# Kernel tuning notes

Measured on AMD Instinct MI355X. Metric: run time of the kernel, lower is better.

The kernel has to match this reference:

```python
import jax, jax.numpy as jnp
import numpy as np

CLASS_NUM = 31
KERNEL_MUL = 2.0
KERNEL_NUM = 5


def setup_inputs() -> dict:
    key = jax.random.key(0)
    k1, k2, k3, k4 = jax.random.split(key, 4)
    B, D = 4096, 512
    source = jax.random.normal(k1, (B, D), dtype=jnp.float32)
    target = jax.random.normal(k2, (B, D), dtype=jnp.float32)
    s_label = jax.random.randint(k3, (B,), 0, CLASS_NUM)
    t_label = jax.random.uniform(k4, (B, CLASS_NUM), dtype=jnp.float32)
    return {"source": source, "target": target, "s_label": s_label, "t_label": t_label}


def _cal_weight(s_label, t_label):
    # Faithful port of the numpy weight computation (detached in the original).
    C = CLASS_NUM
    s_onehot = jax.nn.one_hot(s_label, C, dtype=jnp.float32)          # [Bs, C]
    s_sum = s_onehot.sum(axis=0)
    s_vec = s_onehot / jnp.where(s_sum == 0, 1e9, s_sum)
    t_pred = jnp.argmax(t_label, axis=1)
    t_sum = t_label.sum(axis=0)
    t_vec = t_label / jnp.where(t_sum == 0, 1.0, t_sum)
    # classes present in BOTH source labels and target argmax predictions
    s_present = s_onehot.sum(axis=0) > 0
    t_present = jax.nn.one_hot(t_pred, C, dtype=jnp.float32).sum(axis=0) > 0
    mask = (s_present & t_present).astype(jnp.float32)                # [C]
    s_vec = s_vec * mask
    t_vec = t_vec * mask
    length = mask.sum()
    inv_len = jnp.where(length > 0, 1.0 / length, 0.0)
    w_ss = (s_vec @ s_vec.T) * inv_len
    w_tt = (t_vec @ t_vec.T) * inv_len
    w_st = (s_vec @ t_vec.T) * inv_len
    w_ts = (t_vec @ s_vec.T) * inv_len
    return w_ss, w_tt, w_st, w_ts


def _gaussian_kernel(source, target):
    n = source.shape[0] + target.shape[0]
    total = jnp.concatenate([source, target], axis=0)                 # [n, d]
    # Gram-matrix trick for pairwise squared L2 (avoids n x n x d intermediate)
    sq = jnp.sum(total * total, axis=1)                               # [n]
    L2 = jnp.maximum(sq[:, None] + sq[None, :] - 2.0 * (total @ total.T), 0.0)
    bandwidth = jax.lax.stop_gradient(jnp.sum(L2)) / (n * n - n)      # .data -> detach
    bandwidth = bandwidth / (KERNEL_MUL ** (KERNEL_NUM // 2))
    kernels = jnp.zeros_like(L2)
    for i in range(KERNEL_NUM):
        kernels = kernels + jnp.exp(-L2 / (bandwidth * KERNEL_MUL ** i))
    return kernels


def reference(source, target, s_label, t_label):
    B = source.shape[0]
    w_ss, w_tt, w_st, w_ts = _cal_weight(s_label, t_label)
    w_ss = jax.lax.stop_gradient(w_ss)
    w_tt = jax.lax.stop_gradient(w_tt)
    w_st = jax.lax.stop_gradient(w_st)
    w_ts = jax.lax.stop_gradient(w_ts)
    kernels = _gaussian_kernel(source, target)
    SS = kernels[:B, :B]
    TT = kernels[B:, B:]
    ST = kernels[:B, B:]
    TS = kernels[B:, :B]
    loss = (jnp.sum(w_ss * SS) + jnp.sum(w_tt * TT)
            - jnp.sum(w_st * ST) - jnp.sum(w_ts * TS))
    # original returns 0 if the kernel matrix contains NaNs
    return jnp.where(jnp.any(jnp.isnan(kernels)), 0.0, loss)
```

## Files before the change

### kernel.cpp

```cpp
#include <hip/hip_runtime.h>

#define N_TOT 8192
#define BHALF 4096
#define D 512
#define C 31
#define NKCI 4
#define QS 21.166666666666668f
#define C2 0.0044644089288178575f

typedef float f32x16 __attribute__((ext_vector_type(16)));
typedef int   i32x16 __attribute__((ext_vector_type(16)));
typedef int   i32x4  __attribute__((ext_vector_type(4)));
typedef __bf16 bf16x8 __attribute__((ext_vector_type(8)));

__device__ __forceinline__ uint bf16_rne(uint u) {
  return (u + 0x7fffu + ((u >> 16) & 1u)) >> 16;
}
__device__ __forceinline__ void split2(float x, uint& h, uint& lo) {
  uint u = __float_as_uint(x);
  h = bf16_rne(u);
  float hf = __uint_as_float(h << 16);
  lo = bf16_rne(__float_as_uint(x - hf));
}
__device__ __forceinline__ void gll16(const void* g, void* s) {
  __builtin_amdgcn_global_load_lds(
      (const __attribute__((address_space(1))) unsigned int*)g,
      (__attribute__((address_space(3))) unsigned int*)s, 16, 0, 0);
}
__device__ __forceinline__ uint pack4(const float* x, int o) {
  uint r = 0;
  #pragma unroll
  for (int b = 0; b < 4; ++b) {
    float xs = x[o + b] * QS;
    xs = fmaxf(fminf(xs, 127.f), -127.f);
    int q = __float2int_rn(xs);
    r |= (uint)(q & 255) << (8 * b);
  }
  return r;
}

__global__ __launch_bounds__(256) void k_split(const float* __restrict__ src,
                                               const float* __restrict__ tgt,
                                               const float* __restrict__ tl,
                                               uchar* __restrict__ qG,
                                               float* __restrict__ sq,
                                               float* __restrict__ m,
                                               float* __restrict__ tsum,
                                               int* __restrict__ pres) {
  __shared__ float lsq[4][32];
  __shared__ float lcol[128];
  __shared__ float ts[C];
  int tid = threadIdx.x, l = tid & 63, wid = tid >> 6;
  int bx = (int)blockIdx.x;
  if (bx < 1024) {
    int rg = bx >> 2;
    int kb = bx & 3;
    int ksg = kb * 4 + wid;
    int row = rg * 32 + (l & 31);
    int k0 = ksg * 32 + (l >> 5) * 16;
    const float* p = (row < BHALF) ? src + (size_t)row * D : tgt + (size_t)(row - BHALF) * D;
    float x[16];
    #pragma unroll
    for (int q = 0; q < 4; ++q) {
      float4 v = *(const float4*)(p + k0 + q * 4);
      x[q*4+0] = v.x; x[q*4+1] = v.y; x[q*4+2] = v.z; x[q*4+3] = v.w;
    }
    uint4 o = make_uint4(pack4(x, 0), pack4(x, 4), pack4(x, 8), pack4(x, 12));
    *(uint4*)(qG + (((size_t)rg * 16 + ksg) * 64 + l) * 16) = o;
    float s = 0.f;
    #pragma unroll
    for (int j = 0; j < 16; ++j) s = fmaf(x[j], x[j], s);
    s += __shfl_xor(s, 32);
    if (l < 32) lsq[wid][l] = s;
    #pragma unroll
    for (int off = 1; off <= 16; off <<= 1)
      #pragma unroll
      for (int j = 0; j < 16; ++j) x[j] += __shfl_xor(x[j], off);
    if ((l & 31) == 0) {
      #pragma unroll
      for (int j = 0; j < 16; ++j) lcol[wid * 32 + (l >> 5) * 16 + j] = x[j];
    }
    __syncthreads();
    if (tid < 32) {
      float t = lsq[0][tid] + lsq[1][tid] + lsq[2][tid] + lsq[3][tid];
      atomicAdd(&sq[rg * 32 + tid], t);
    } else if (tid >= 128) {
      int cc = tid - 128;
      atomicAdd(&m[kb * 128 + cc], lcol[cc]);
    }
  } else {
    int b = bx - 1024;
    if (tid < C) ts[tid] = 0.f;
    __syncthreads();
    int base = b * 128 * C;
    for (int idx = tid; idx < 128 * C; idx += 256) {
      atomicAdd(&ts[idx % C], tl[base + idx]);
    }
    if (tid < 128) {
      int row = b * 128 + tid;
      const float* p = tl + (size_t)row * C;
      float best = p[0]; int bi = 0;
      for (int c = 1; c < C; c++) { float v = p[c]; if (v > best) { best = v; bi = c; } }
      pres[bi] = 1;
    }
    __syncthreads();
    if (tid < C) atomicAdd(&tsum[tid], ts[tid]);
  }
}

__global__ __launch_bounds__(256) void k_prep(const float* __restrict__ sq,
                                              const float* __restrict__ m,
                                              const int* __restrict__ slab,
                                              const float* __restrict__ tsum,
                                              const int* __restrict__ pres,
                                              float* __restrict__ sval,
                                              float* __restrict__ tscale,
                                              float* __restrict__ scal,
                                              float* __restrict__ out) {
  __shared__ float red[4];
  __shared__ int cnt[C];
  __shared__ float Ssh, Msh;
  int tid = threadIdx.x;
  if (tid < C) cnt[tid] = 0;
  float s = 0.f;
  for (int i = tid; i < N_TOT; i += 256) s += sq[i];
  #pragma unroll
  for (int off = 32; off; off >>= 1) s += __shfl_xor(s, off);
  if ((tid & 63) == 0) red[tid >> 6] = s;
  __syncthreads();
  if (tid == 0) Ssh = red[0] + red[1] + red[2] + red[3];
  __syncthreads();
  float q = 0.f;
  for (int d = tid; d < D; d += 256) q += m[d] * m[d];
  #pragma unroll
  for (int off = 32; off; off >>= 1) q += __shfl_xor(q, off);
  if ((tid & 63) == 0) red[tid >> 6] = q;
  __syncthreads();
  if (tid == 0) Msh = red[0] + red[1] + red[2] + red[3];
  for (int i = tid; i < BHALF; i += 256) atomicAdd(&cnt[slab[i]], 1);
  __syncthreads();
  if (tid == 0) {
    double S = (double)Ssh, M2 = (double)Msh;
    double sumL2 = 2.0 * (double)N_TOT * S - 2.0 * M2;
    double bw = sumL2 / ((double)N_TOT * (double)N_TOT - (double)N_TOT) / 4.0;
    scal[0] = (float)(-1.4426950408889634 / (16.0 * bw));
    int len = 0;
    for (int c = 0; c < C; c++) {
      int mk = (cnt[c] > 0 && pres[c] != 0) ? 1 : 0;
      len += mk;
      sval[c] = mk ? (1.0f / (float)cnt[c]) : 0.0f;
      float tv = tsum[c];
      tscale[c] = mk ? (1.0f / (tv == 0.0f ? 1.0f : tv)) : 0.0f;
    }
    scal[1] = (len > 0) ? (1.0f / (float)len) : 0.0f;
    out[0] = 0.f;
  }
}

__global__ __launch_bounds__(256, 4) void k_main(
    const uchar* __restrict__ qG,
    const int* __restrict__ slab, const float* __restrict__ tl,
    const float* __restrict__ sval, const float* __restrict__ tscale,
    const float* __restrict__ sq, const float* __restrict__ scal,
    float* __restrict__ out) {
  __shared__ uint4 As4[1024];
  __shared__ uint4 Bs4[1024];
  __shared__ float sqA[128], sqB[128], red[4];
  uchar* As = (uchar*)As4;
  uchar* Bs = (uchar*)Bs4;
  ushort* AsU = (ushort*)As4;
  ushort* BsU = (ushort*)Bs4;

  int tid = threadIdx.x;
  int l = tid & 63, wid = tid >> 6;

  int bid = (int)blockIdx.x;
  int swz = (bid & 7) * 260 + (bid >> 3);

  int ti = 0, rem = swz;
  for (;;) { int w = 64 - ti; if (rem < w) break; rem -= w; ++ti; }
  int tj = ti + rem;

  if (tid < 128) { sqA[tid] = sq[ti * 128 + tid]; sqB[tid] = sq[tj * 128 + tid]; }
  float nib = scal[0], invlen = scal[1];

  i32x16 zeroi;
  f32x16 zero16;
  #pragma unroll
  for (int k = 0; k < 16; ++k) { zeroi[k] = 0; zero16[k] = 0.f; }
  i32x16 acc[2][2];
  acc[0][0] = zeroi; acc[0][1] = zeroi; acc[1][0] = zeroi; acc[1][1] = zeroi;

  int wrg = (wid >> 1) * 2;
  int wcg = (wid & 1) * 2;

  int rgbase_m = ((wid < 2) ? ti : tj) * 4;
  int rg_off = (wid & 1) * 2;
  uchar* lb_m = (wid < 2) ? As : Bs;

  for (int kci = 0; kci < NKCI; ++kci) {
    #pragma unroll
    for (int r = 0; r < 8; ++r) {
      int rgl = rg_off + (r >> 2), ksl = r & 3;
      const uchar* g = qG + (((size_t)(rgbase_m + rgl) * 16 + kci * 4 + ksl) * 64 + l) * 16;
      gll16(g, lb_m + ((rgl * 4 + ksl) * 64 + l) * 16);
    }
    __syncthreads();
    __builtin_amdgcn_s_setprio(1);
    #pragma unroll
    for (int ksl = 0; ksl < 4; ++ksl) {
      i32x4 a0 = *(const i32x4*)(As + (((wrg + 0) * 4 + ksl) * 64 + l) * 16);
      i32x4 a1 = *(const i32x4*)(As + (((wrg + 1) * 4 + ksl) * 64 + l) * 16);
      i32x4 b0 = *(const i32x4*)(Bs + (((wcg + 0) * 4 + ksl) * 64 + l) * 16);
      i32x4 b1 = *(const i32x4*)(Bs + (((wcg + 1) * 4 + ksl) * 64 + l) * 16);
      acc[0][0] = __builtin_amdgcn_mfma_i32_32x32x32_i8(a0, b0, acc[0][0], 0, 0, 0);
      acc[0][1] = __builtin_amdgcn_mfma_i32_32x32x32_i8(a0, b1, acc[0][1], 0, 0, 0);
      acc[1][0] = __builtin_amdgcn_mfma_i32_32x32x32_i8(a1, b0, acc[1][0], 0, 0, 0);
      acc[1][1] = __builtin_amdgcn_mfma_i32_32x32x32_i8(a1, b1, acc[1][1], 0, 0, 0);
    }
    __builtin_amdgcn_s_setprio(0);
    __syncthreads();
  }

  #pragma unroll
  for (int it = 0; it < 4; ++it) {
    int slot = tid + it * 256;
    int pl = slot >> 6;
    int ll = slot & 63;
    int side = pl >> 3;
    int rgl = (pl & 7) >> 1;
    int ks = pl & 1;
    int row = (side ? tj : ti) * 128 + rgl * 32 + (ll & 31);
    int j0 = ks * 16 + (ll >> 5) * 8;
    float vals[8];
    if (row < BHALF) {
      int cls = slab[row];
      float v = sval[cls];
      #pragma unroll
      for (int jj = 0; jj < 8; ++jj) vals[jj] = (j0 + jj == cls) ? v : 0.f;
    } else {
      const float* p = tl + (size_t)(row - BHALF) * C;
      #pragma unroll
      for (int jj = 0; jj < 8; ++jj) {
        int cj = j0 + jj;
        vals[jj] = (cj < C) ? -p[cj] * tscale[cj] : 0.f;
      }
    }
    uint h[8], lo[8];
    #pragma unroll
    for (int jj = 0; jj < 8; ++jj) split2(vals[jj], h[jj], lo[jj]);
    ushort* base = (side ? BsU : AsU) + ((rgl * 2 + ks) * 64 + ll) * 8;
    *(uint4*)base = make_uint4(h[0]|(h[1]<<16), h[2]|(h[3]<<16),
                               h[4]|(h[5]<<16), h[6]|(h[7]<<16));
    *(uint4*)(base + 4096) = make_uint4(lo[0]|(lo[1]<<16), lo[2]|(lo[3]<<16),
                                        lo[4]|(lo[5]<<16), lo[6]|(lo[7]<<16));
  }
  __syncthreads();

  float partial = 0.f;
  int colb = (wid & 1) * 64 + (l & 31);
  int rowb = (wid >> 1) * 64 + 4 * (l >> 5);
  #pragma unroll
  for (int i = 0; i < 2; ++i) {
    bf16x8 caH0 = *(const bf16x8*)(AsU + (((wrg + i) * 2 + 0) * 64 + l) * 8);
    bf16x8 caH1 = *(const bf16x8*)(AsU + (((wrg + i) * 2 + 1) * 64 + l) * 8);
    bf16x8 caL0 = *(const bf16x8*)(AsU + 4096 + (((wrg + i) * 2 + 0) * 64 + l) * 8);
    bf16x8 caL1 = *(const bf16x8*)(AsU + 4096 + (((wrg + i) * 2 + 1) * 64 + l) * 8);
    #pragma unroll
    for (int j = 0; j < 2; ++j) {
      bf16x8 cbH0 = *(const bf16x8*)(BsU + (((wcg + j) * 2 + 0) * 64 + l) * 8);
      bf16x8 cbH1 = *(const bf16x8*)(BsU + (((wcg + j) * 2 + 1) * 64 + l) * 8);
      bf16x8 cbL0 = *(const bf16x8*)(BsU + 4096 + (((wcg + j) * 2 + 0) * 64 + l) * 8);
      bf16x8 cbL1 = *(const bf16x8*)(BsU + 4096 + (((wcg + j) * 2 + 1) * 64 + l) * 8);
      f32x16 w = zero16;
      w = __builtin_amdgcn_mfma_f32_32x32x16_bf16(caH0, cbH0, w, 0, 0, 0);
      w = __builtin_amdgcn_mfma_f32_32x32x16_bf16(caH1, cbH1, w, 0, 0, 0);
      w = __builtin_amdgcn_mfma_f32_32x32x16_bf16(caH0, cbL0, w, 0, 0, 0);
      w = __builtin_amdgcn_mfma_f32_32x32x16_bf16(caH1, cbL1, w, 0, 0, 0);
      w = __builtin_amdgcn_mfma_f32_32x32x16_bf16(caL0, cbH0, w, 0, 0, 0);
      w = __builtin_amdgcn_mfma_f32_32x32x16_bf16(caL1, cbH1, w, 0, 0, 0);
      float sb = sqB[colb + j * 32];
      #pragma unroll
      for (int reg = 0; reg < 16; ++reg) {
        int row = rowb + i * 32 + (reg & 3) + 8 * (reg >> 2);
        float l2 = fmaxf(sqA[row] + sb - C2 * (float)acc[i][j][reg], 0.f);
        float e = __builtin_amdgcn_exp2f(l2 * nib);
        float kern = e;
        e *= e; kern += e;
        e *= e; kern += e;
        e *= e; kern += e;
        e *= e; kern += e;
        partial = fmaf(w[reg], kern, partial);
      }
    }
  }
  #pragma unroll
  for (int off = 32; off; off >>= 1) partial += __shfl_xor(partial, off);
  if (l == 0) red[wid] = partial;
  __syncthreads();
  if (tid == 0) {
    float v = (red[0] + red[1] + red[2] + red[3]) * invlen * ((ti == tj) ? 1.0f : 2.0f);
    atomicAdd(out, v);
  }
}

extern "C" void kernel_launch(void* const* d_in, const int* in_sizes, int n_in,
                              void* d_out, int out_size, void* d_ws, size_t ws_size,
                              hipStream_t stream) {
  const float* src = (const float*)d_in[0];
  const float* tgt = (const float*)d_in[1];
  const int* slab  = (const int*)d_in[2];
  const float* tl  = (const float*)d_in[3];
  float* out = (float*)d_out;

  uchar*  qG = (uchar*)d_ws;
  float* fb  = (float*)(qG + 4194304);
  float* sq     = fb;
  float* m      = fb + 8192;
  float* tsum   = fb + 8704;
  int*   pres   = (int*)(fb + 8736);
  float* sval   = fb + 8768;
  float* tscale = fb + 8800;
  float* scal   = fb + 8832;

  hipMemsetAsync(fb, 0, 8864 * sizeof(float), stream);
  hipLaunchKernelGGL(k_split, dim3(1056), dim3(256), 0, stream,
                     src, tgt, tl, qG, sq, m, tsum, pres);
  hipLaunchKernelGGL(k_prep,  dim3(1),    dim3(256), 0, stream,
                     sq, m, slab, tsum, pres, sval, tscale, scal, out);
  hipLaunchKernelGGL(k_main,  dim3(2080), dim3(256), 0, stream,
                     qG, slab, tl, sval, tscale, sq, scal, out);
}
```

Measured before the change: 93.76 us.

## Double-buffer k_main loads and fold prep kernel into split and main

Removes the single-block k_prep launch: class counts move into k_split's label blocks, and every k_main block recomputes the bandwidth and class weights redundantly after its GEMM loop. The K loop of k_main now uses two LDS buffers with smaller k-steps, issuing the next stage's async global-to-LDS loads before computing on the current one, with explicit vmcnt waits and raw barriers instead of __syncthreads. This is meant to hide load latency and cut one serial launch. In exchange each of the 2080 blocks rereads and reduces the 8192-entry sq array and the m vector.

```diff
diff --git a/kernel.cpp b/kernel.cpp
--- a/kernel.cpp
+++ b/kernel.cpp
@@ -4,7 +4,6 @@
 #define BHALF 4096
 #define D 512
 #define C 31
-#define NKCI 4
 #define QS 21.166666666666668f
 #define C2 0.0044644089288178575f
 
@@ -42,14 +41,18 @@
 __global__ __launch_bounds__(256) void k_split(const float* __restrict__ src,
                                                const float* __restrict__ tgt,
                                                const float* __restrict__ tl,
+                                               const int* __restrict__ slab,
                                                uchar* __restrict__ qG,
                                                float* __restrict__ sq,
                                                float* __restrict__ m,
                                                float* __restrict__ tsum,
-                                               int* __restrict__ pres) {
+                                               int* __restrict__ pres,
+                                               int* __restrict__ cnt,
+                                               float* __restrict__ out) {
   __shared__ float lsq[4][32];
   __shared__ float lcol[128];
   __shared__ float ts[C];
+  __shared__ int hcnt[C];
   int tid = threadIdx.x, l = tid & 63, wid = tid >> 6;
   int bx = (int)blockIdx.x;
   if (bx < 1024) {
@@ -90,7 +93,7 @@
     }
   } else {
     int b = bx - 1024;
-    if (tid < C) ts[tid] = 0.f;
+    if (tid < C) { ts[tid] = 0.f; hcnt[tid] = 0; }
     __syncthreads();
     int base = b * 128 * C;
     for (int idx = tid; idx < 128 * C; idx += 256) {
@@ -102,88 +105,40 @@
       float best = p[0]; int bi = 0;
       for (int c = 1; c < C; c++) { float v = p[c]; if (v > best) { best = v; bi = c; } }
       pres[bi] = 1;
-    }
+      atomicAdd(&hcnt[slab[row]], 1);
+    }
+    if (b == 0 && tid == 255) out[0] = 0.f;
     __syncthreads();
-    if (tid < C) atomicAdd(&tsum[tid], ts[tid]);
-  }
-}
-
-__global__ __launch_bounds__(256) void k_prep(const float* __restrict__ sq,
-                                              const float* __restrict__ m,
-                                              const int* __restrict__ slab,
-                                              const float* __restrict__ tsum,
-                                              const int* __restrict__ pres,
-                                              float* __restrict__ sval,
-                                              float* __restrict__ tscale,
-                                              float* __restrict__ scal,
-                                              float* __restrict__ out) {
-  __shared__ float red[4];
-  __shared__ int cnt[C];
-  __shared__ float Ssh, Msh;
-  int tid = threadIdx.x;
-  if (tid < C) cnt[tid] = 0;
-  float s = 0.f;
-  for (int i = tid; i < N_TOT; i += 256) s += sq[i];
-  #pragma unroll
-  for (int off = 32; off; off >>= 1) s += __shfl_xor(s, off);
-  if ((tid & 63) == 0) red[tid >> 6] = s;
-  __syncthreads();
-  if (tid == 0) Ssh = red[0] + red[1] + red[2] + red[3];
-  __syncthreads();
-  float q = 0.f;
-  for (int d = tid; d < D; d += 256) q += m[d] * m[d];
-  #pragma unroll
-  for (int off = 32; off; off >>= 1) q += __shfl_xor(q, off);
-  if ((tid & 63) == 0) red[tid >> 6] = q;
-  __syncthreads();
-  if (tid == 0) Msh = red[0] + red[1] + red[2] + red[3];
-  for (int i = tid; i < BHALF; i += 256) atomicAdd(&cnt[slab[i]], 1);
-  __syncthreads();
-  if (tid == 0) {
-    double S = (double)Ssh, M2 = (double)Msh;
-    double sumL2 = 2.0 * (double)N_TOT * S - 2.0 * M2;
-    double bw = sumL2 / ((double)N_TOT * (double)N_TOT - (double)N_TOT) / 4.0;
-    scal[0] = (float)(-1.4426950408889634 / (16.0 * bw));
-    int len = 0;
-    for (int c = 0; c < C; c++) {
-      int mk = (cnt[c] > 0 && pres[c] != 0) ? 1 : 0;
-      len += mk;
-      sval[c] = mk ? (1.0f / (float)cnt[c]) : 0.0f;
-      float tv = tsum[c];
-      tscale[c] = mk ? (1.0f / (tv == 0.0f ? 1.0f : tv)) : 0.0f;
-    }
-    scal[1] = (len > 0) ? (1.0f / (float)len) : 0.0f;
-    out[0] = 0.f;
-  }
-}
+    if (tid < C) {
+      atomicAdd(&tsum[tid], ts[tid]);
+      atomicAdd(&cnt[tid], hcnt[tid]);
+    }
+  }
+}
+
+#define WAITV4 asm volatile("s_waitcnt vmcnt(4)" ::: "memory")
+#define WAITV0 asm volatile("s_waitcnt vmcnt(0)" ::: "memory")
+#define WAITL0 asm volatile("s_waitcnt lgkmcnt(0)" ::: "memory")
 
 __global__ __launch_bounds__(256, 4) void k_main(
     const uchar* __restrict__ qG,
     const int* __restrict__ slab, const float* __restrict__ tl,
-    const float* __restrict__ sval, const float* __restrict__ tscale,
-    const float* __restrict__ sq, const float* __restrict__ scal,
-    float* __restrict__ out) {
-  __shared__ uint4 As4[1024];
-  __shared__ uint4 Bs4[1024];
-  __shared__ float sqA[128], sqB[128], red[4];
-  uchar* As = (uchar*)As4;
-  uchar* Bs = (uchar*)Bs4;
-  ushort* AsU = (ushort*)As4;
-  ushort* BsU = (ushort*)Bs4;
+    const float* __restrict__ sq, const float* __restrict__ m,
+    const float* __restrict__ tsum, const int* __restrict__ pres,
+    const int* __restrict__ cnt, float* __restrict__ out) {
+  __shared__ uint4 lds4[2][1024];
+  __shared__ float sqA[128], sqB[128], red[8];
+  __shared__ float svalS[32], tscaleS[32], scalS[1];
 
   int tid = threadIdx.x;
   int l = tid & 63, wid = tid >> 6;
 
   int bid = (int)blockIdx.x;
   int swz = (bid & 7) * 260 + (bid >> 3);
-
   int ti = 0, rem = swz;
   for (;;) { int w = 64 - ti; if (rem < w) break; rem -= w; ++ti; }
   int tj = ti + rem;
 
-  if (tid < 128) { sqA[tid] = sq[ti * 128 + tid]; sqB[tid] = sq[tj * 128 + tid]; }
-  float nib = scal[0], invlen = scal[1];
-
   i32x16 zeroi;
   f32x16 zero16;
   #pragma unroll
@@ -196,32 +151,75 @@
 
   int rgbase_m = ((wid < 2) ? ti : tj) * 4;
   int rg_off = (wid & 1) * 2;
-  uchar* lb_m = (wid < 2) ? As : Bs;
-
-  for (int kci = 0; kci < NKCI; ++kci) {
-    #pragma unroll
-    for (int r = 0; r < 8; ++r) {
-      int rgl = rg_off + (r >> 2), ksl = r & 3;
-      const uchar* g = qG + (((size_t)(rgbase_m + rgl) * 16 + kci * 4 + ksl) * 64 + l) * 16;
-      gll16(g, lb_m + ((rgl * 4 + ksl) * 64 + l) * 16);
-    }
-    __syncthreads();
+  int side_off = (wid < 2) ? 0 : 8192;
+
+#define STAGE(P) do {                                                              \
+    uchar* lb = ((uchar*)lds4[(P) & 1]) + side_off;                                \
+    _Pragma("unroll")                                                              \
+    for (int r = 0; r < 4; ++r) {                                                  \
+      int rgl = rg_off + (r >> 1), ksl = r & 1;                                    \
+      const uchar* g = qG + (((size_t)(rgbase_m + rgl) * 16 + ((P) * 2 + ksl)) * 64 + l) * 16; \
+      gll16(g, lb + ((rgl * 2 + ksl) * 64 + l) * 16);                              \
+    }                                                                              \
+  } while (0)
+
+  STAGE(0);
+  #pragma unroll
+  for (int p = 0; p < 8; ++p) {
+    if (p + 1 < 8) STAGE(p + 1);
+    if (p < 7) { WAITV4; } else { WAITV0; }
+    __builtin_amdgcn_sched_barrier(0);
+    __builtin_amdgcn_s_barrier();
+    uchar* As = (uchar*)lds4[p & 1];
+    uchar* Bs = As + 8192;
     __builtin_amdgcn_s_setprio(1);
     #pragma unroll
-    for (int ksl = 0; ksl < 4; ++ksl) {
-      i32x4 a0 = *(const i32x4*)(As + (((wrg + 0) * 4 + ksl) * 64 + l) * 16);
-      i32x4 a1 = *(const i32x4*)(As + (((wrg + 1) * 4 + ksl) * 64 + l) * 16);
-      i32x4 b0 = *(const i32x4*)(Bs + (((wcg + 0) * 4 + ksl) * 64 + l) * 16);
-      i32x4 b1 = *(const i32x4*)(Bs + (((wcg + 1) * 4 + ksl) * 64 + l) * 16);
+    for (int ksl = 0; ksl < 2; ++ksl) {
+      i32x4 a0 = *(const i32x4*)(As + (((wrg + 0) * 2 + ksl) * 64 + l) * 16);
+      i32x4 a1 = *(const i32x4*)(As + (((wrg + 1) * 2 + ksl) * 64 + l) * 16);
+      i32x4 b0 = *(const i32x4*)(Bs + (((wcg + 0) * 2 + ksl) * 64 + l) * 16);
+      i32x4 b1 = *(const i32x4*)(Bs + (((wcg + 1) * 2 + ksl) * 64 + l) * 16);
       acc[0][0] = __builtin_amdgcn_mfma_i32_32x32x32_i8(a0, b0, acc[0][0], 0, 0, 0);
       acc[0][1] = __builtin_amdgcn_mfma_i32_32x32x32_i8(a0, b1, acc[0][1], 0, 0, 0);
       acc[1][0] = __builtin_amdgcn_mfma_i32_32x32x32_i8(a1, b0, acc[1][0], 0, 0, 0);
       acc[1][1] = __builtin_amdgcn_mfma_i32_32x32x32_i8(a1, b1, acc[1][1], 0, 0, 0);
     }
     __builtin_amdgcn_s_setprio(0);
-    __syncthreads();
-  }
-
+    WAITL0;
+    __builtin_amdgcn_sched_barrier(0);
+    __builtin_amdgcn_s_barrier();
+  }
+#undef STAGE
+
+  if (tid < 128) { sqA[tid] = sq[ti * 128 + tid]; sqB[tid] = sq[tj * 128 + tid]; }
+  float s = 0.f;
+  for (int i = tid; i < N_TOT; i += 256) s += sq[i];
+  float q = 0.f;
+  for (int d = tid; d < D; d += 256) q += m[d] * m[d];
+  #pragma unroll
+  for (int off = 32; off; off >>= 1) { s += __shfl_xor(s, off); q += __shfl_xor(q, off); }
+  if (l == 0) { red[wid] = s; red[4 + wid] = q; }
+  __syncthreads();
+  float Ssum = red[0] + red[1] + red[2] + red[3];
+  float Msum = red[4] + red[5] + red[6] + red[7];
+  double sumL2 = 2.0 * (double)N_TOT * (double)Ssum - 2.0 * (double)Msum;
+  double bw = sumL2 / ((double)N_TOT * (double)N_TOT - (double)N_TOT) / 4.0;
+  float nib = (float)(-1.4426950408889634 / (16.0 * bw));
+  if (tid < 32) {
+    int c = tid;
+    int cc = 0; float tv = 0.f; int pr = 0;
+    if (c < C) { cc = cnt[c]; tv = tsum[c]; pr = pres[c]; }
+    int mk = (cc > 0 && pr != 0) ? 1 : 0;
+    unsigned long long ball = __ballot(mk);
+    int len = __popcll(ball);
+    svalS[c] = mk ? (1.0f / (float)cc) : 0.f;
+    tscaleS[c] = mk ? (1.0f / (tv == 0.f ? 1.f : tv)) : 0.f;
+    if (c == 0) scalS[0] = (len > 0) ? (1.0f / (float)len) : 0.f;
+  }
+  __syncthreads();
+
+  ushort* AsU = (ushort*)lds4[0];
+  ushort* BsU = (ushort*)lds4[1];
   #pragma unroll
   for (int it = 0; it < 4; ++it) {
     int slot = tid + it * 256;
@@ -235,7 +233,7 @@
     float vals[8];
     if (row < BHALF) {
       int cls = slab[row];
-      float v = sval[cls];
+      float v = svalS[cls];
       #pragma unroll
       for (int jj = 0; jj < 8; ++jj) vals[jj] = (j0 + jj == cls) ? v : 0.f;
     } else {
@@ -243,7 +241,7 @@
       #pragma unroll
       for (int jj = 0; jj < 8; ++jj) {
         int cj = j0 + jj;
-        vals[jj] = (cj < C) ? -p[cj] * tscale[cj] : 0.f;
+        vals[jj] = (cj < C) ? -p[cj] * tscaleS[cj] : 0.f;
       }
     }
     uint h[8], lo[8];
@@ -299,7 +297,7 @@
   if (l == 0) red[wid] = partial;
   __syncthreads();
   if (tid == 0) {
-    float v = (red[0] + red[1] + red[2] + red[3]) * invlen * ((ti == tj) ? 1.0f : 2.0f);
+    float v = (red[0] + red[1] + red[2] + red[3]) * scalS[0] * ((ti == tj) ? 1.0f : 2.0f);
     atomicAdd(out, v);
   }
 }
@@ -315,19 +313,15 @@
 
   uchar*  qG = (uchar*)d_ws;
   float* fb  = (float*)(qG + 4194304);
-  float* sq     = fb;
-  float* m      = fb + 8192;
-  float* tsum   = fb + 8704;
-  int*   pres   = (int*)(fb + 8736);
-  float* sval   = fb + 8768;
-  float* tscale = fb + 8800;
-  float* scal   = fb + 8832;
-
-  hipMemsetAsync(fb, 0, 8864 * sizeof(float), stream);
+  float* sq   = fb;
+  float* m    = fb + 8192;
+  float* tsum = fb + 8704;
+  int*   pres = (int*)(fb + 8736);
+  int*   cnt  = (int*)(fb + 8768);
+
+  hipMemsetAsync(fb, 0, 8800 * sizeof(float), stream);
   hipLaunchKernelGGL(k_split, dim3(1056), dim3(256), 0, stream,
-                     src, tgt, tl, qG, sq, m, tsum, pres);
-  hipLaunchKernelGGL(k_prep,  dim3(1),    dim3(256), 0, stream,
-                     sq, m, slab, tsum, pres, sval, tscale, scal, out);
+                     src, tgt, tl, slab, qG, sq, m, tsum, pres, cnt, out);
   hipLaunchKernelGGL(k_main,  dim3(2080), dim3(256), 0, stream,
-                     qG, slab, tl, sval, tscale, sq, scal, out);
-}
+                     qG, slab, tl, sq, m, tsum, pres, cnt, out);
+}
```

Measured after the change: 89.36 us. 4.7% less time.

## Load int8 GEMM operands directly from global memory into registers, skipping LDS staging

Applied to the files above, without the earlier changes.

The k_main int8 Gram-matrix loop no longer stages A/B tiles through LDS with global_load_lds and barriers. Each wave now reads its pre-swizzled MFMA fragments straight from global memory over all 16 k-steps, with no __syncthreads in the loop. Occupancy hint drops from 4 to 2 blocks per CU, and the memset size shrinks. Each tile is now fetched by two waves instead of once per block, so cache traffic rises, in exchange for fewer barriers and less LDS latency.

```diff
diff --git a/kernel.cpp b/kernel.cpp
--- a/kernel.cpp
+++ b/kernel.cpp
@@ -4,7 +4,6 @@
 #define BHALF 4096
 #define D 512
 #define C 31
-#define NKCI 4
 #define QS 21.166666666666668f
 #define C2 0.0044644089288178575f
 
@@ -21,11 +20,6 @@
   h = bf16_rne(u);
   float hf = __uint_as_float(h << 16);
   lo = bf16_rne(__float_as_uint(x - hf));
-}
-__device__ __forceinline__ void gll16(const void* g, void* s) {
-  __builtin_amdgcn_global_load_lds(
-      (const __attribute__((address_space(1))) unsigned int*)g,
-      (__attribute__((address_space(3))) unsigned int*)s, 16, 0, 0);
 }
 __device__ __forceinline__ uint pack4(const float* x, int o) {
   uint r = 0;
@@ -157,7 +151,7 @@
   }
 }
 
-__global__ __launch_bounds__(256, 4) void k_main(
+__global__ __launch_bounds__(256, 2) void k_main(
     const uchar* __restrict__ qG,
     const int* __restrict__ slab, const float* __restrict__ tl,
     const float* __restrict__ sval, const float* __restrict__ tscale,
@@ -166,8 +160,6 @@
   __shared__ uint4 As4[1024];
   __shared__ uint4 Bs4[1024];
   __shared__ float sqA[128], sqB[128], red[4];
-  uchar* As = (uchar*)As4;
-  uchar* Bs = (uchar*)Bs4;
   ushort* AsU = (ushort*)As4;
   ushort* BsU = (ushort*)Bs4;
 
@@ -176,13 +168,11 @@
 
   int bid = (int)blockIdx.x;
   int swz = (bid & 7) * 260 + (bid >> 3);
-
   int ti = 0, rem = swz;
   for (;;) { int w = 64 - ti; if (rem < w) break; rem -= w; ++ti; }
   int tj = ti + rem;
 
   if (tid < 128) { sqA[tid] = sq[ti * 128 + tid]; sqB[tid] = sq[tj * 128 + tid]; }
-  float nib = scal[0], invlen = scal[1];
 
   i32x16 zeroi;
   f32x16 zero16;
@@ -194,32 +184,20 @@
   int wrg = (wid >> 1) * 2;
   int wcg = (wid & 1) * 2;
 
-  int rgbase_m = ((wid < 2) ? ti : tj) * 4;
-  int rg_off = (wid & 1) * 2;
-  uchar* lb_m = (wid < 2) ? As : Bs;
-
-  for (int kci = 0; kci < NKCI; ++kci) {
-    #pragma unroll
-    for (int r = 0; r < 8; ++r) {
-      int rgl = rg_off + (r >> 2), ksl = r & 3;
-      const uchar* g = qG + (((size_t)(rgbase_m + rgl) * 16 + kci * 4 + ksl) * 64 + l) * 16;
-      gll16(g, lb_m + ((rgl * 4 + ksl) * 64 + l) * 16);
-    }
-    __syncthreads();
-    __builtin_amdgcn_s_setprio(1);
-    #pragma unroll
-    for (int ksl = 0; ksl < 4; ++ksl) {
-      i32x4 a0 = *(const i32x4*)(As + (((wrg + 0) * 4 + ksl) * 64 + l) * 16);
-      i32x4 a1 = *(const i32x4*)(As + (((wrg + 1) * 4 + ksl) * 64 + l) * 16);
-      i32x4 b0 = *(const i32x4*)(Bs + (((wcg + 0) * 4 + ksl) * 64 + l) * 16);
-      i32x4 b1 = *(const i32x4*)(Bs + (((wcg + 1) * 4 + ksl) * 64 + l) * 16);
-      acc[0][0] = __builtin_amdgcn_mfma_i32_32x32x32_i8(a0, b0, acc[0][0], 0, 0, 0);
-      acc[0][1] = __builtin_amdgcn_mfma_i32_32x32x32_i8(a0, b1, acc[0][1], 0, 0, 0);
-      acc[1][0] = __builtin_amdgcn_mfma_i32_32x32x32_i8(a1, b0, acc[1][0], 0, 0, 0);
-      acc[1][1] = __builtin_amdgcn_mfma_i32_32x32x32_i8(a1, b1, acc[1][1], 0, 0, 0);
-    }
-    __builtin_amdgcn_s_setprio(0);
-    __syncthreads();
+  const uchar* pA0 = qG + ((size_t)(ti * 4 + wrg + 0) * 16 * 64 + l) * 16;
+  const uchar* pA1 = qG + ((size_t)(ti * 4 + wrg + 1) * 16 * 64 + l) * 16;
+  const uchar* pB0 = qG + ((size_t)(tj * 4 + wcg + 0) * 16 * 64 + l) * 16;
+  const uchar* pB1 = qG + ((size_t)(tj * 4 + wcg + 1) * 16 * 64 + l) * 16;
+  #pragma unroll
+  for (int ksg = 0; ksg < 16; ++ksg) {
+    i32x4 a0 = *(const i32x4*)(pA0 + ksg * 1024);
+    i32x4 a1 = *(const i32x4*)(pA1 + ksg * 1024);
+    i32x4 b0 = *(const i32x4*)(pB0 + ksg * 1024);
+    i32x4 b1 = *(const i32x4*)(pB1 + ksg * 1024);
+    acc[0][0] = __builtin_amdgcn_mfma_i32_32x32x32_i8(a0, b0, acc[0][0], 0, 0, 0);
+    acc[0][1] = __builtin_amdgcn_mfma_i32_32x32x32_i8(a0, b1, acc[0][1], 0, 0, 0);
+    acc[1][0] = __builtin_amdgcn_mfma_i32_32x32x32_i8(a1, b0, acc[1][0], 0, 0, 0);
+    acc[1][1] = __builtin_amdgcn_mfma_i32_32x32x32_i8(a1, b1, acc[1][1], 0, 0, 0);
   }
 
   #pragma unroll
@@ -257,6 +235,7 @@
   }
   __syncthreads();
 
+  float nib = scal[0], invlen = scal[1];
   float partial = 0.f;
   int colb = (wid & 1) * 64 + (l & 31);
   int rowb = (wid >> 1) * 64 + 4 * (l >> 5);
@@ -323,7 +302,7 @@
   float* tscale = fb + 8800;
   float* scal   = fb + 8832;
 
-  hipMemsetAsync(fb, 0, 8864 * sizeof(float), stream);
+  hipMemsetAsync(fb, 0, 8768 * sizeof(float), stream);
   hipLaunchKernelGGL(k_split, dim3(1056), dim3(256), 0, stream,
                      src, tgt, tl, qG, sq, m, tsum, pres);
   hipLaunchKernelGGL(k_prep,  dim3(1),    dim3(256), 0, stream,
```

New measurement: 90.49 us. -3.5%, faster.

## Double-buffer int8 K-chunks in LDS to overlap global loads with MFMA

Applied to the files above, without the earlier changes.

The main k_main GEMM loop now splits K into 8 smaller chunks held in two LDS buffers. The next chunk is prefetched with direct-to-LDS loads while the current one is consumed, using explicit vmcnt waits and raw barriers in place of a full sync after each load. Occupancy hint drops from 4 to 3 blocks per CU, but LDS per block stays the same. The memset size is trimmed and the scalar loads move later in the kernel, both minor.

```diff
diff --git a/kernel.cpp b/kernel.cpp
--- a/kernel.cpp
+++ b/kernel.cpp
@@ -4,7 +4,6 @@
 #define BHALF 4096
 #define D 512
 #define C 31
-#define NKCI 4
 #define QS 21.166666666666668f
 #define C2 0.0044644089288178575f
 
@@ -157,32 +156,31 @@
   }
 }
 
-__global__ __launch_bounds__(256, 4) void k_main(
+#define WAITV4 asm volatile("s_waitcnt vmcnt(4)" ::: "memory")
+#define WAITV0 asm volatile("s_waitcnt vmcnt(0)" ::: "memory")
+#define WAITL0 asm volatile("s_waitcnt lgkmcnt(0)" ::: "memory")
+
+__global__ __launch_bounds__(256, 3) void k_main(
     const uchar* __restrict__ qG,
     const int* __restrict__ slab, const float* __restrict__ tl,
     const float* __restrict__ sval, const float* __restrict__ tscale,
     const float* __restrict__ sq, const float* __restrict__ scal,
     float* __restrict__ out) {
-  __shared__ uint4 As4[1024];
-  __shared__ uint4 Bs4[1024];
+  __shared__ uint4 lds4[2][1024];
   __shared__ float sqA[128], sqB[128], red[4];
-  uchar* As = (uchar*)As4;
-  uchar* Bs = (uchar*)Bs4;
-  ushort* AsU = (ushort*)As4;
-  ushort* BsU = (ushort*)Bs4;
+  ushort* AsU = (ushort*)lds4[0];
+  ushort* BsU = (ushort*)lds4[1];
 
   int tid = threadIdx.x;
   int l = tid & 63, wid = tid >> 6;
 
   int bid = (int)blockIdx.x;
   int swz = (bid & 7) * 260 + (bid >> 3);
-
   int ti = 0, rem = swz;
   for (;;) { int w = 64 - ti; if (rem < w) break; rem -= w; ++ti; }
   int tj = ti + rem;
 
   if (tid < 128) { sqA[tid] = sq[ti * 128 + tid]; sqB[tid] = sq[tj * 128 + tid]; }
-  float nib = scal[0], invlen = scal[1];
 
   i32x16 zeroi;
   f32x16 zero16;
@@ -196,31 +194,43 @@
 
   int rgbase_m = ((wid < 2) ? ti : tj) * 4;
   int rg_off = (wid & 1) * 2;
-  uchar* lb_m = (wid < 2) ? As : Bs;
-
-  for (int kci = 0; kci < NKCI; ++kci) {
-    #pragma unroll
-    for (int r = 0; r < 8; ++r) {
-      int rgl = rg_off + (r >> 2), ksl = r & 3;
-      const uchar* g = qG + (((size_t)(rgbase_m + rgl) * 16 + kci * 4 + ksl) * 64 + l) * 16;
-      gll16(g, lb_m + ((rgl * 4 + ksl) * 64 + l) * 16);
-    }
-    __syncthreads();
+  int side_off = (wid < 2) ? 0 : 8192;
+
+#define STAGE(P) do {                                                              \
+    uchar* lb = ((uchar*)lds4[(P) & 1]) + side_off;                                \
+    _Pragma("unroll")                                                              \
+    for (int r = 0; r < 4; ++r) {                                                  \
+      int rgl = rg_off + (r >> 1), ksl = r & 1;                                    \
+      const uchar* g = qG + (((size_t)(rgbase_m + rgl) * 16 + ((P) * 2 + ksl)) * 64 + l) * 16; \
+      gll16(g, lb + ((rgl * 2 + ksl) * 64 + l) * 16);                              \
+    }                                                                              \
+  } while (0)
+
+  STAGE(0);
+  #pragma unroll
+  for (int p = 0; p < 8; ++p) {
+    if (p + 1 < 8) STAGE(p + 1);
+    if (p < 7) { WAITV4; } else { WAITV0; }
+    __builtin_amdgcn_s_barrier();
+    uchar* As = (uchar*)lds4[p & 1];
+    uchar* Bs = As + 8192;
     __builtin_amdgcn_s_setprio(1);
     #pragma unroll
-    for (int ksl = 0; ksl < 4; ++ksl) {
-      i32x4 a0 = *(const i32x4*)(As + (((wrg + 0) * 4 + ksl) * 64 + l) * 16);
-      i32x4 a1 = *(const i32x4*)(As + (((wrg + 1) * 4 + ksl) * 64 + l) * 16);
-      i32x4 b0 = *(const i32x4*)(Bs + (((wcg + 0) * 4 + ksl) * 64 + l) * 16);
-      i32x4 b1 = *(const i32x4*)(Bs + (((wcg + 1) * 4 + ksl) * 64 + l) * 16);
+    for (int ksl = 0; ksl < 2; ++ksl) {
+      i32x4 a0 = *(const i32x4*)(As + (((wrg + 0) * 2 + ksl) * 64 + l) * 16);
+      i32x4 a1 = *(const i32x4*)(As + (((wrg + 1) * 2 + ksl) * 64 + l) * 16);
+      i32x4 b0 = *(const i32x4*)(Bs + (((wcg + 0) * 2 + ksl) * 64 + l) * 16);
+      i32x4 b1 = *(const i32x4*)(Bs + (((wcg + 1) * 2 + ksl) * 64 + l) * 16);
       acc[0][0] = __builtin_amdgcn_mfma_i32_32x32x32_i8(a0, b0, acc[0][0], 0, 0, 0);
       acc[0][1] = __builtin_amdgcn_mfma_i32_32x32x32_i8(a0, b1, acc[0][1], 0, 0, 0);
       acc[1][0] = __builtin_amdgcn_mfma_i32_32x32x32_i8(a1, b0, acc[1][0], 0, 0, 0);
       acc[1][1] = __builtin_amdgcn_mfma_i32_32x32x32_i8(a1, b1, acc[1][1], 0, 0, 0);
     }
     __builtin_amdgcn_s_setprio(0);
-    __syncthreads();
-  }
+    WAITL0;
+    __builtin_amdgcn_s_barrier();
+  }
+#undef STAGE
 
   #pragma unroll
   for (int it = 0; it < 4; ++it) {
@@ -257,6 +267,7 @@
   }
   __syncthreads();
 
+  float nib = scal[0], invlen = scal[1];
   float partial = 0.f;
   int colb = (wid & 1) * 64 + (l & 31);
   int rowb = (wid >> 1) * 64 + 4 * (l >> 5);
@@ -323,7 +334,7 @@
   float* tscale = fb + 8800;
   float* scal   = fb + 8832;
 
-  hipMemsetAsync(fb, 0, 8864 * sizeof(float), stream);
+  hipMemsetAsync(fb, 0, 8768 * sizeof(float), stream);
   hipLaunchKernelGGL(k_split, dim3(1056), dim3(256), 0, stream,
                      src, tgt, tl, qG, sq, m, tsum, pres);
   hipLaunchKernelGGL(k_prep,  dim3(1),    dim3(256), 0, stream,
```

Measured after the change: 90.78 us. -3.2%, faster.
